# Performance work log

Hardware: AMD Instinct MI355X
Metric: run time of the kernel (lower is better)

The kernel has to match this reference:

```python
import jax, jax.numpy as jnp
import numpy as np

B, S, D, U = 64, 2048, 512, 512

def setup_inputs() -> dict:
    key = jax.random.key(0)
    ks = jax.random.split(key, 8)
    query = jax.random.normal(ks[0], (B, D), dtype=jnp.float32)
    values = jax.random.normal(ks[1], (B, S, D), dtype=jnp.float32)
    # Keras Dense params (glorot-like scale), with biases (Dense default use_bias=True)
    W1 = jax.random.normal(ks[2], (D, U), dtype=jnp.float32) / np.sqrt(D)
    b1 = jnp.zeros((U,), dtype=jnp.float32)
    W2 = jax.random.normal(ks[3], (D, U), dtype=jnp.float32) / np.sqrt(D)
    b2 = jnp.zeros((U,), dtype=jnp.float32)
    V = jax.random.normal(ks[4], (U, 1), dtype=jnp.float32) / np.sqrt(U)
    bv = jnp.zeros((1,), dtype=jnp.float32)
    return {"query": query, "values": values, "W1": W1, "b1": b1,
            "W2": W2, "b2": b2, "V": V, "bv": bv}

def reference(query, values, W1, b1, W2, b2, V, bv) -> jnp.ndarray:
    # query: [B, D], values: [B, S, D]
    q_proj = query @ W1 + b1                      # [B, U]
    v_proj = jnp.einsum('bsd,du->bsu', values, W2) + b2  # [B, S, U]
    h = jnp.tanh(q_proj[:, None, :] + v_proj)     # [B, S, U]
    scores = jnp.einsum('bsu,uo->bso', h, V) + bv # [B, S, 1]
    attn = jax.nn.softmax(scores, axis=1)         # softmax over sequence axis
    context = jnp.sum(attn * values, axis=1)      # [B, D]
    return context
```

## Files before the change

### kernel.cpp

```cpp
#include <hip/hip_runtime.h>
#include <hip/hip_bf16.h>

#define BB 64
#define SS 2048
#define DD 512
#define UU 512
#define BS (BB*SS)

typedef __attribute__((ext_vector_type(8))) short bf16x8;
typedef __attribute__((ext_vector_type(16))) float f32x16;

static __device__ __forceinline__ unsigned short f2bf(float x) {
    union { float f; unsigned int u; } v; v.f = x;
    unsigned int r = v.u + 0x7FFFu + ((v.u >> 16) & 1u);
    return (unsigned short)(r >> 16);
}

__global__ void k_prep(const float* __restrict__ W2, unsigned short* __restrict__ W2F,
                       const float* __restrict__ query, const float* __restrict__ W1,
                       const float* __restrict__ b1, const float* __restrict__ b2,
                       float* __restrict__ qpb) {
    __shared__ float tile[64][65];
    const int t = threadIdx.x;
    if (blockIdx.x < 64) {
        const int ti = blockIdx.x >> 3;
        const int tj = blockIdx.x & 7;
        #pragma unroll
        for (int i = 0; i < 16; ++i) {
            int e = i*256 + t;
            int dr = e >> 6, uc = e & 63;
            tile[dr][uc] = W2[(size_t)(ti*64+dr)*UU + tj*64+uc];
        }
        __syncthreads();
        const int ksl = t >> 6, ln = t & 63;
        const int lh = ln >> 5, l31 = ln & 31;
        #pragma unroll
        for (int ntl = 0; ntl < 2; ++ntl) {
            const int ks = ti*4 + ksl;
            const int ntile = tj*2 + ntl;
            bf16x8 g;
            #pragma unroll
            for (int j = 0; j < 8; ++j)
                g[j] = (short)f2bf(tile[ksl*16 + lh*8 + j][ntl*32 + l31]);
            *(bf16x8*)&W2F[(size_t)(((ks*16 + ntile)*64 + ln) * 8)] = g;
        }
    } else {
        const int b = blockIdx.x - 64;
        float a0 = 0.f, a1 = 0.f;
        for (int d = 0; d < DD; ++d) {
            float q = query[b*DD + d];
            a0 += q * W1[(size_t)d*UU + t];
            a1 += q * W1[(size_t)d*UU + t + 256];
        }
        qpb[b*UU + t]       = a0 + b1[t]     + b2[t];
        qpb[b*UU + t + 256] = a1 + b1[t+256] + b2[t+256];
    }
}

__launch_bounds__(256, 2)
__global__ void k_scores(const float* __restrict__ values,
                         const unsigned short* __restrict__ W2F,
                         const float* __restrict__ qpb,
                         const float* __restrict__ Vw,
                         float* __restrict__ pm, float* __restrict__ pl,
                         float* __restrict__ pv) {
    __shared__ unsigned short Albuf[64*512];
    const int t   = threadIdx.x;
    const int blk = blockIdx.x;
    const int m0  = blk * 64;
    const int b   = blk >> 5;
    const int wave = t >> 6, lane = t & 63;
    const int ln31 = lane & 31, half = lane >> 5;

    const bf16x8* Bp = (const bf16x8*)W2F;
    bf16x8 bfr[2][4];
    #pragma unroll
    for (int nt = 0; nt < 4; ++nt)
        bfr[0][nt] = Bp[(0*16 + wave*4 + nt)*64 + lane];
    #pragma unroll
    for (int nt = 0; nt < 4; ++nt)
        bfr[1][nt] = Bp[(1*16 + wave*4 + nt)*64 + lane];

    float qv[4], vw[4];
    #pragma unroll
    for (int nt = 0; nt < 4; ++nt) {
        int n = wave*128 + nt*32 + ln31;
        qv[nt] = qpb[b*UU + n];
        vw[nt] = Vw[n];
    }

    const float* src = values + (size_t)m0 * DD;
    #pragma unroll
    for (int i = 0; i < 16; ++i) {
        int gf  = i*256 + t;
        int row = gf >> 6;
        int g   = gf & 63;
        const float4 f0 = *(const float4*)(src + (size_t)row*DD + g*8);
        const float4 f1 = *(const float4*)(src + (size_t)row*DD + g*8 + 4);
        bf16x8 pk;
        pk[0] = (short)f2bf(f0.x); pk[1] = (short)f2bf(f0.y);
        pk[2] = (short)f2bf(f0.z); pk[3] = (short)f2bf(f0.w);
        pk[4] = (short)f2bf(f1.x); pk[5] = (short)f2bf(f1.y);
        pk[6] = (short)f2bf(f1.z); pk[7] = (short)f2bf(f1.w);
        *(bf16x8*)&Albuf[row*512 + ((g ^ (row & 7)) << 3)] = pk;
    }
    __syncthreads();

    f32x16 acc[2][4];
    #pragma unroll
    for (int mt = 0; mt < 2; ++mt)
        #pragma unroll
        for (int nt = 0; nt < 4; ++nt)
            #pragma unroll
            for (int r = 0; r < 16; ++r)
                acc[mt][nt][r] = 0.f;

    const int xm = ln31 & 7;
    #pragma unroll 4
    for (int ks = 0; ks < 32; ++ks) {
        const int cur = ks & 1;
        const int g8 = (((ks*2 + half) ^ xm) << 3);
        bf16x8 a0 = *(const bf16x8*)&Albuf[ln31*512 + g8];
        bf16x8 a1 = *(const bf16x8*)&Albuf[16384 + ln31*512 + g8];
        #pragma unroll
        for (int nt = 0; nt < 4; ++nt) {
            acc[0][nt] = __builtin_amdgcn_mfma_f32_32x32x16_bf16(a0, bfr[cur][nt], acc[0][nt], 0, 0, 0);
            acc[1][nt] = __builtin_amdgcn_mfma_f32_32x32x16_bf16(a1, bfr[cur][nt], acc[1][nt], 0, 0, 0);
        }
        #pragma unroll
        for (int nt = 0; nt < 4; ++nt)
            bfr[cur][nt] = Bp[((ks+2)*16 + wave*4 + nt)*64 + lane];
    }

    float sacc[2][16];
    #pragma unroll
    for (int mt = 0; mt < 2; ++mt)
        #pragma unroll
        for (int r = 0; r < 16; ++r)
            sacc[mt][r] = 0.f;
    #pragma unroll
    for (int nt = 0; nt < 4; ++nt) {
        const float q = qv[nt], w = vw[nt];
        #pragma unroll
        for (int mt = 0; mt < 2; ++mt)
            #pragma unroll
            for (int r = 0; r < 16; ++r) {
                float x = q + acc[mt][nt][r];
                float e = __expf(x + x);
                float rc = __builtin_amdgcn_rcpf(e + 1.f);
                sacc[mt][r] = fmaf(fmaf(-2.f, rc, 1.f), w, sacc[mt][r]);
            }
    }

    __syncthreads();
    float* sred = (float*)Albuf;
    #pragma unroll
    for (int mt = 0; mt < 2; ++mt)
        #pragma unroll
        for (int r = 0; r < 16; ++r) {
            float v = sacc[mt][r];
            v += __shfl_xor(v, 1);
            v += __shfl_xor(v, 2);
            v += __shfl_xor(v, 4);
            v += __shfl_xor(v, 8);
            v += __shfl_xor(v, 16);
            if (ln31 == 0)
                sred[wave*64 + mt*32 + (r & 3) + 8*(r >> 2) + 4*half] = v;
        }
    __syncthreads();

    if (t < 64) {
        float s = sred[t] + sred[64 + t] + sred[128 + t] + sred[192 + t];
        float m = s;
        #pragma unroll
        for (int off = 32; off; off >>= 1) m = fmaxf(m, __shfl_xor(m, off));
        float p = __expf(s - m);
        float l = p;
        #pragma unroll
        for (int off = 32; off; off >>= 1) l += __shfl_xor(l, off);
        sred[256 + t] = p;
        if (t == 0) { pm[blk] = m; pl[blk] = l; }
    }
    __syncthreads();

    float2 cacc = make_float2(0.f, 0.f);
    const float* vrow = values + (size_t)m0*DD + t*2;
    #pragma unroll 8
    for (int i = 0; i < 64; ++i) {
        float p = sred[256 + i];
        float2 v = *(const float2*)(vrow + (size_t)i*DD);
        cacc.x = fmaf(p, v.x, cacc.x);
        cacc.y = fmaf(p, v.y, cacc.y);
    }
    *(float2*)&pv[(size_t)blk*DD + t*2] = cacc;
}

__global__ void k_finish(const float* __restrict__ pv, const float* __restrict__ pm,
                         const float* __restrict__ pl, float* __restrict__ out) {
    __shared__ float sm_[32], sl_[32], sw[32];
    const int b = blockIdx.x, t = threadIdx.x;
    if (t < 32) { sm_[t] = pm[b*32 + t]; sl_[t] = pl[b*32 + t]; }
    __syncthreads();
    float M = -1e30f;
    #pragma unroll
    for (int c = 0; c < 32; ++c) M = fmaxf(M, sm_[c]);
    float L = 0.f;
    #pragma unroll
    for (int c = 0; c < 32; ++c) L += sl_[c] * __expf(sm_[c] - M);
    if (t < 32) sw[t] = __expf(sm_[t] - M) / L;
    __syncthreads();
    float2 a = make_float2(0.f, 0.f);
    #pragma unroll 4
    for (int c = 0; c < 32; ++c) {
        float w = sw[c];
        float2 v = *(const float2*)&pv[(size_t)(b*32 + c)*DD + t*2];
        a.x = fmaf(w, v.x, a.x);
        a.y = fmaf(w, v.y, a.y);
    }
    *(float2*)&out[(size_t)b*DD + t*2] = a;
}

extern "C" void kernel_launch(void* const* d_in, const int* in_sizes, int n_in,
                              void* d_out, int out_size, void* d_ws, size_t ws_size,
                              hipStream_t stream) {
    const float* query  = (const float*)d_in[0];
    const float* values = (const float*)d_in[1];
    const float* W1     = (const float*)d_in[2];
    const float* b1     = (const float*)d_in[3];
    const float* W2     = (const float*)d_in[4];
    const float* b2     = (const float*)d_in[5];
    const float* Vw     = (const float*)d_in[6];

    char* ws = (char*)d_ws;
    unsigned short* W2F = (unsigned short*)ws;
    float* qpb = (float*)(ws + 557056);
    float* pm  = (float*)(ws + 557056 + 131072);
    float* pl  = (float*)(ws + 557056 + 131072 + 8192);
    float* pv  = (float*)(ws + 557056 + 131072 + 16384);

    k_prep<<<128, 256, 0, stream>>>(W2, W2F, query, W1, b1, b2, qpb);
    k_scores<<<BS/64, 256, 0, stream>>>(values, W2F, qpb, Vw, pm, pl, pv);
    k_finish<<<BB, 256, 0, stream>>>(pv, pm, pl, (float*)d_out);
}
```

Measured before the change: 510.1 us.

## Process score tiles in two 32-row halves to shrink LDS and raise occupancy

The scores kernel now converts and multiplies its 64-row block as two sequential 32-row halves. This halves the shared-memory tile and lets the launch bound request 5 blocks per CU instead of 2, in exchange for re-streaming the W2 fragments once per half. The B-fragment prefetch ring is deepened to 4 slots, and the workspace offsets move so the larger over-read past the end of W2F stays in bounds. The finish kernel is split over 4 blocks per batch with a shuffle-based max/sum, and the query projection uses extra independent accumulators; the tight register budget risks spills.

```diff
diff --git a/kernel.cpp b/kernel.cpp
--- a/kernel.cpp
+++ b/kernel.cpp
@@ -46,40 +46,34 @@
         }
     } else {
         const int b = blockIdx.x - 64;
-        float a0 = 0.f, a1 = 0.f;
-        for (int d = 0; d < DD; ++d) {
-            float q = query[b*DD + d];
-            a0 += q * W1[(size_t)d*UU + t];
-            a1 += q * W1[(size_t)d*UU + t + 256];
-        }
-        qpb[b*UU + t]       = a0 + b1[t]     + b2[t];
-        qpb[b*UU + t + 256] = a1 + b1[t+256] + b2[t+256];
-    }
-}
-
-__launch_bounds__(256, 2)
+        float a0 = 0.f, a1 = 0.f, a2 = 0.f, a3 = 0.f;
+        for (int d = 0; d < DD; d += 2) {
+            float q0 = query[b*DD + d], q1 = query[b*DD + d + 1];
+            a0 = fmaf(q0, W1[(size_t)d*UU + t], a0);
+            a1 = fmaf(q1, W1[(size_t)(d+1)*UU + t], a1);
+            a2 = fmaf(q0, W1[(size_t)d*UU + t + 256], a2);
+            a3 = fmaf(q1, W1[(size_t)(d+1)*UU + t + 256], a3);
+        }
+        qpb[b*UU + t]       = a0 + a1 + b1[t]     + b2[t];
+        qpb[b*UU + t + 256] = a2 + a3 + b1[t+256] + b2[t+256];
+    }
+}
+
+__launch_bounds__(256, 5)
 __global__ void k_scores(const float* __restrict__ values,
                          const unsigned short* __restrict__ W2F,
                          const float* __restrict__ qpb,
                          const float* __restrict__ Vw,
                          float* __restrict__ pm, float* __restrict__ pl,
                          float* __restrict__ pv) {
-    __shared__ unsigned short Albuf[64*512];
+    __shared__ unsigned short Albuf[32*512];
     const int t   = threadIdx.x;
     const int blk = blockIdx.x;
     const int m0  = blk * 64;
     const int b   = blk >> 5;
     const int wave = t >> 6, lane = t & 63;
     const int ln31 = lane & 31, half = lane >> 5;
-
-    const bf16x8* Bp = (const bf16x8*)W2F;
-    bf16x8 bfr[2][4];
-    #pragma unroll
-    for (int nt = 0; nt < 4; ++nt)
-        bfr[0][nt] = Bp[(0*16 + wave*4 + nt)*64 + lane];
-    #pragma unroll
-    for (int nt = 0; nt < 4; ++nt)
-        bfr[1][nt] = Bp[(1*16 + wave*4 + nt)*64 + lane];
+    const int xm = ln31 & 7;
 
     float qv[4], vw[4];
     #pragma unroll
@@ -89,83 +83,86 @@
         vw[nt] = Vw[n];
     }
 
-    const float* src = values + (size_t)m0 * DD;
-    #pragma unroll
-    for (int i = 0; i < 16; ++i) {
-        int gf  = i*256 + t;
-        int row = gf >> 6;
-        int g   = gf & 63;
-        const float4 f0 = *(const float4*)(src + (size_t)row*DD + g*8);
-        const float4 f1 = *(const float4*)(src + (size_t)row*DD + g*8 + 4);
-        bf16x8 pk;
-        pk[0] = (short)f2bf(f0.x); pk[1] = (short)f2bf(f0.y);
-        pk[2] = (short)f2bf(f0.z); pk[3] = (short)f2bf(f0.w);
-        pk[4] = (short)f2bf(f1.x); pk[5] = (short)f2bf(f1.y);
-        pk[6] = (short)f2bf(f1.z); pk[7] = (short)f2bf(f1.w);
-        *(bf16x8*)&Albuf[row*512 + ((g ^ (row & 7)) << 3)] = pk;
-    }
-    __syncthreads();
-
-    f32x16 acc[2][4];
-    #pragma unroll
-    for (int mt = 0; mt < 2; ++mt)
-        #pragma unroll
-        for (int nt = 0; nt < 4; ++nt)
-            #pragma unroll
-            for (int r = 0; r < 16; ++r)
-                acc[mt][nt][r] = 0.f;
-
-    const int xm = ln31 & 7;
-    #pragma unroll 4
-    for (int ks = 0; ks < 32; ++ks) {
-        const int cur = ks & 1;
-        const int g8 = (((ks*2 + half) ^ xm) << 3);
-        bf16x8 a0 = *(const bf16x8*)&Albuf[ln31*512 + g8];
-        bf16x8 a1 = *(const bf16x8*)&Albuf[16384 + ln31*512 + g8];
-        #pragma unroll
-        for (int nt = 0; nt < 4; ++nt) {
-            acc[0][nt] = __builtin_amdgcn_mfma_f32_32x32x16_bf16(a0, bfr[cur][nt], acc[0][nt], 0, 0, 0);
-            acc[1][nt] = __builtin_amdgcn_mfma_f32_32x32x16_bf16(a1, bfr[cur][nt], acc[1][nt], 0, 0, 0);
-        }
-        #pragma unroll
-        for (int nt = 0; nt < 4; ++nt)
-            bfr[cur][nt] = Bp[((ks+2)*16 + wave*4 + nt)*64 + lane];
-    }
-
+    const bf16x8* Bp = (const bf16x8*)W2F;
     float sacc[2][16];
     #pragma unroll
-    for (int mt = 0; mt < 2; ++mt)
+    for (int tau = 0; tau < 2; ++tau)
         #pragma unroll
         for (int r = 0; r < 16; ++r)
-            sacc[mt][r] = 0.f;
-    #pragma unroll
-    for (int nt = 0; nt < 4; ++nt) {
-        const float q = qv[nt], w = vw[nt];
-        #pragma unroll
-        for (int mt = 0; mt < 2; ++mt)
+            sacc[tau][r] = 0.f;
+
+    for (int tau = 0; tau < 2; ++tau) {
+        const float* src = values + (size_t)(m0 + tau*32) * DD;
+        #pragma unroll
+        for (int i = 0; i < 8; ++i) {
+            int gf  = i*256 + t;
+            int row = gf >> 6;
+            int g   = gf & 63;
+            const float4 f0 = *(const float4*)(src + (size_t)row*DD + g*8);
+            const float4 f1 = *(const float4*)(src + (size_t)row*DD + g*8 + 4);
+            bf16x8 pk;
+            pk[0] = (short)f2bf(f0.x); pk[1] = (short)f2bf(f0.y);
+            pk[2] = (short)f2bf(f0.z); pk[3] = (short)f2bf(f0.w);
+            pk[4] = (short)f2bf(f1.x); pk[5] = (short)f2bf(f1.y);
+            pk[6] = (short)f2bf(f1.z); pk[7] = (short)f2bf(f1.w);
+            *(bf16x8*)&Albuf[row*512 + ((g ^ (row & 7)) << 3)] = pk;
+        }
+
+        bf16x8 bfr[4][4];
+        #pragma unroll
+        for (int p = 0; p < 4; ++p)
+            #pragma unroll
+            for (int nt = 0; nt < 4; ++nt)
+                bfr[p][nt] = Bp[(p*16 + wave*4 + nt)*64 + lane];
+
+        __syncthreads();
+
+        f32x16 acc[4];
+        #pragma unroll
+        for (int nt = 0; nt < 4; ++nt)
+            #pragma unroll
+            for (int r = 0; r < 16; ++r)
+                acc[nt][r] = 0.f;
+
+        #pragma unroll 4
+        for (int ks = 0; ks < 32; ++ks) {
+            const int slot = ks & 3;
+            bf16x8 a0 = *(const bf16x8*)&Albuf[ln31*512 + (((ks*2 + half) ^ xm) << 3)];
+            #pragma unroll
+            for (int nt = 0; nt < 4; ++nt)
+                acc[nt] = __builtin_amdgcn_mfma_f32_32x32x16_bf16(a0, bfr[slot][nt], acc[nt], 0, 0, 0);
+            #pragma unroll
+            for (int nt = 0; nt < 4; ++nt)
+                bfr[slot][nt] = Bp[((ks+4)*16 + wave*4 + nt)*64 + lane];
+        }
+
+        #pragma unroll
+        for (int nt = 0; nt < 4; ++nt) {
+            const float q = qv[nt], w = vw[nt];
             #pragma unroll
             for (int r = 0; r < 16; ++r) {
-                float x = q + acc[mt][nt][r];
+                float x = q + acc[nt][r];
                 float e = __expf(x + x);
                 float rc = __builtin_amdgcn_rcpf(e + 1.f);
-                sacc[mt][r] = fmaf(fmaf(-2.f, rc, 1.f), w, sacc[mt][r]);
+                sacc[tau][r] = fmaf(fmaf(-2.f, rc, 1.f), w, sacc[tau][r]);
             }
-    }
-
-    __syncthreads();
+        }
+        __syncthreads();
+    }
+
     float* sred = (float*)Albuf;
     #pragma unroll
-    for (int mt = 0; mt < 2; ++mt)
+    for (int tau = 0; tau < 2; ++tau)
         #pragma unroll
         for (int r = 0; r < 16; ++r) {
-            float v = sacc[mt][r];
+            float v = sacc[tau][r];
             v += __shfl_xor(v, 1);
             v += __shfl_xor(v, 2);
             v += __shfl_xor(v, 4);
             v += __shfl_xor(v, 8);
             v += __shfl_xor(v, 16);
             if (ln31 == 0)
-                sred[wave*64 + mt*32 + (r & 3) + 8*(r >> 2) + 4*half] = v;
+                sred[wave*64 + tau*32 + (r & 3) + 8*(r >> 2) + 4*half] = v;
         }
     __syncthreads();
 
@@ -197,27 +194,28 @@
 
 __global__ void k_finish(const float* __restrict__ pv, const float* __restrict__ pm,
                          const float* __restrict__ pl, float* __restrict__ out) {
-    __shared__ float sm_[32], sl_[32], sw[32];
-    const int b = blockIdx.x, t = threadIdx.x;
-    if (t < 32) { sm_[t] = pm[b*32 + t]; sl_[t] = pl[b*32 + t]; }
+    __shared__ float sw[32];
+    const int b = blockIdx.x >> 2, d0 = (blockIdx.x & 3) * 128;
+    const int t = threadIdx.x;
+    if (t < 32) {
+        float m = pm[b*32 + t], l = pl[b*32 + t];
+        float M = m;
+        #pragma unroll
+        for (int off = 16; off; off >>= 1) M = fmaxf(M, __shfl_xor(M, off));
+        float le = l * __expf(m - M);
+        float L = le;
+        #pragma unroll
+        for (int off = 16; off; off >>= 1) L += __shfl_xor(L, off);
+        sw[t] = __expf(m - M) / L;
+    }
     __syncthreads();
-    float M = -1e30f;
-    #pragma unroll
-    for (int c = 0; c < 32; ++c) M = fmaxf(M, sm_[c]);
-    float L = 0.f;
-    #pragma unroll
-    for (int c = 0; c < 32; ++c) L += sl_[c] * __expf(sm_[c] - M);
-    if (t < 32) sw[t] = __expf(sm_[t] - M) / L;
-    __syncthreads();
-    float2 a = make_float2(0.f, 0.f);
-    #pragma unroll 4
-    for (int c = 0; c < 32; ++c) {
-        float w = sw[c];
-        float2 v = *(const float2*)&pv[(size_t)(b*32 + c)*DD + t*2];
-        a.x = fmaf(w, v.x, a.x);
-        a.y = fmaf(w, v.y, a.y);
-    }
-    *(float2*)&out[(size_t)b*DD + t*2] = a;
+    if (t < 128) {
+        float a = 0.f;
+        #pragma unroll 4
+        for (int c = 0; c < 32; ++c)
+            a = fmaf(sw[c], pv[(size_t)(b*32 + c)*DD + d0 + t], a);
+        out[(size_t)b*DD + d0 + t] = a;
+    }
 }
 
 extern "C" void kernel_launch(void* const* d_in, const int* in_sizes, int n_in,
@@ -233,12 +231,12 @@
 
     char* ws = (char*)d_ws;
     unsigned short* W2F = (unsigned short*)ws;
-    float* qpb = (float*)(ws + 557056);
-    float* pm  = (float*)(ws + 557056 + 131072);
-    float* pl  = (float*)(ws + 557056 + 131072 + 8192);
-    float* pv  = (float*)(ws + 557056 + 131072 + 16384);
+    float* qpb = (float*)(ws + 589824);
+    float* pm  = (float*)(ws + 589824 + 131072);
+    float* pl  = (float*)(ws + 589824 + 131072 + 8192);
+    float* pv  = (float*)(ws + 589824 + 131072 + 16384);
 
     k_prep<<<128, 256, 0, stream>>>(W2, W2F, query, W1, b1, b2, qpb);
     k_scores<<<BS/64, 256, 0, stream>>>(values, W2F, qpb, Vw, pm, pl, pv);
-    k_finish<<<BB, 256, 0, stream>>>(pv, pm, pl, (float*)d_out);
-}
+    k_finish<<<BB*4, 256, 0, stream>>>(pv, pm, pl, (float*)d_out);
+}
```

After: 1.326 ms. 2.6x slower.
